# Kernel optimization log

Hardware: AMD Instinct MI355X
Metric: run time of the kernel (lower is better)

The kernel has to match this reference:

```python
import jax, jax.numpy as jnp
import numpy as np

B, S, D, V = 2, 2048, 4096, 32000

def setup_inputs() -> dict:
    key = jax.random.key(0)
    k1, k2, k3 = jax.random.split(key, 3)
    hidden_states = jax.random.normal(k1, (B, S, D), dtype=jnp.float32)
    W = jax.random.normal(k2, (V, D), dtype=jnp.float32) * 0.02  # lm_head weight [vocab, hidden]
    label_ids = jax.random.randint(k3, (B, S), 0, V, dtype=jnp.int64)
    return {"hidden_states": hidden_states, "W": W, "label_ids": label_ids}

def reference(hidden_states, W, label_ids):
    # lm_head: Linear(D, V, bias=False) -> logits [B, S, V], cast to fp32
    logits = jnp.einsum('bsd,vd->bsv', hidden_states, W).astype(jnp.float32)
    # shift: predict token t+1 from position t
    shift_logits = logits[:, :-1, :].reshape(-1, V)          # [B*(S-1), V]
    shift_labels = label_ids[:, 1:].reshape(-1)              # [B*(S-1)]
    logp = jax.nn.log_softmax(shift_logits, axis=-1)
    nll = -jnp.take_along_axis(logp, shift_labels[:, None], axis=1)[:, 0]
    loss = jnp.mean(nll)  # CrossEntropyLoss default reduction='mean'
    return loss, logits
```

## Files before the change

kernel.cpp:

```cpp
#include <hip/hip_runtime.h>
#include <hip/hip_bf16.h>

#define M_ 4096
#define N_ 32000
#define K_ 4096
#define S_ 2048
#define SM1 2047
#define NROWS 4094
#define NT_ 64
#define NB_ 125

typedef __bf16 bf16x8 __attribute__((ext_vector_type(8)));
typedef float f32x4 __attribute__((ext_vector_type(4)));

#define GLDS16(g, l)                                                         \
  __builtin_amdgcn_global_load_lds(                                          \
      (__attribute__((address_space(1))) const void*)(g),                    \
      (__attribute__((address_space(3))) void*)(l), 16, 0, 0)
#define BAR() __builtin_amdgcn_s_barrier()
#define PRIO1() __builtin_amdgcn_s_setprio(1)
#define PRIO0() __builtin_amdgcn_s_setprio(0)
#define VMCNT(n) asm volatile("s_waitcnt vmcnt(" #n ")" ::: "memory")

__global__ __launch_bounds__(256) void cvt_f32_to_bf16(
    const float* __restrict__ in, bf16x8* __restrict__ out, long n8) {
  long i0 = (long)blockIdx.x * blockDim.x + threadIdx.x;
  long stride = (long)gridDim.x * blockDim.x;
  for (long i = i0; i < n8; i += stride) {
    const float4* p = reinterpret_cast<const float4*>(in) + i * 2;
    float4 a = p[0];
    float4 b = p[1];
    bf16x8 v;
    v[0] = (__bf16)a.x; v[1] = (__bf16)a.y; v[2] = (__bf16)a.z; v[3] = (__bf16)a.w;
    v[4] = (__bf16)b.x; v[5] = (__bf16)b.y; v[6] = (__bf16)b.z; v[7] = (__bf16)b.w;
    out[i] = v;
  }
}

__global__ __launch_bounds__(512, 2) void gemm256(
    const __bf16* __restrict__ A, const __bf16* __restrict__ B,
    float* __restrict__ C, float* __restrict__ pm, float* __restrict__ ps) {
  __shared__ __align__(1024) unsigned char smem[2][65536];

  const int tid = threadIdx.x;
  const int bid = blockIdx.x;
  const int wg = (bid & 7) * 250 + (bid >> 3);
  const int nblk = wg >> 4;
  const int mblk = wg & 15;
  const int m0 = mblk * 256;
  const int n0 = nblk * 256;

  const int w = tid >> 6;
  const int lane = tid & 63;
  const int wm = w >> 2;
  const int wn = w & 3;
  const int rl = lane & 15;
  const int cl = lane >> 4;
  const int srow = tid >> 3;
  const int scc = tid & 7;

  f32x4 acc[8][4];
#pragma unroll
  for (int i = 0; i < 8; ++i)
#pragma unroll
    for (int j = 0; j < 4; ++j) acc[i][j] = (f32x4){0.f, 0.f, 0.f, 0.f};

  auto stA2 = [&](int nbuf, int kt, int q) {
#pragma unroll
    for (int j = 0; j < 2; ++j) {
      const int r0 = q * 64 + j * 128;
      const int row = r0 + srow;
      const int c = scc ^ (row & 7);
      GLDS16(A + (size_t)(m0 + row) * K_ + kt * 64 + c * 8,
             &smem[nbuf][r0 * 128 + tid * 16]);
    }
  };
  auto stB2 = [&](int nbuf, int kt, int q) {
#pragma unroll
    for (int j = 0; j < 2; ++j) {
      const int cg = j * 512 + tid;
      const int rl_ = cg >> 3;
      const int row = ((rl_ >> 5) << 6) + q * 32 + (rl_ & 31);
      const int cc = cg & 7;
      const int c = cc ^ (row & 7);
      GLDS16(B + (size_t)(n0 + row) * K_ + kt * 64 + c * 8,
             &smem[nbuf][32768 + row * 128 + cc * 16]);
    }
  };
  auto ld = [&](const unsigned char* base, int row, int c) -> bf16x8 {
    return *(const bf16x8*)(base + row * 128 + (((c ^ row) & 7) << 4));
  };

  stA2(0, 0, 0); stB2(0, 0, 0); stA2(0, 0, 1); stB2(0, 0, 1);
  VMCNT(4);
  BAR();

  bf16x8 al[4][2], ah[4][2], b0r[2][2], b1r[2][2];
#pragma unroll
  for (int jj = 0; jj < 2; ++jj)
#pragma unroll
    for (int ks = 0; ks < 2; ++ks)
      b0r[jj][ks] = ld(smem[0] + 32768, wn * 64 + jj * 16 + rl, ks * 4 + cl);
#pragma unroll
  for (int ii = 0; ii < 4; ++ii)
#pragma unroll
    for (int ks = 0; ks < 2; ++ks)
      al[ii][ks] = ld(smem[0], wm * 128 + ii * 16 + rl, ks * 4 + cl);

  for (int s = 0; s < NT_; ++s) {
    const int cur = s & 1;
    const int nxt = cur ^ 1;
    const unsigned char* bA = smem[cur];
    const unsigned char* bB = smem[cur] + 32768;
    const bool st = (s + 1 < NT_);

    if (st) stA2(nxt, s + 1, 0);
    PRIO1();
#pragma unroll
    for (int ii = 0; ii < 4; ++ii)
#pragma unroll
      for (int jj = 0; jj < 2; ++jj)
#pragma unroll
        for (int ks = 0; ks < 2; ++ks)
          acc[ii][jj] = __builtin_amdgcn_mfma_f32_16x16x32_bf16(
              al[ii][ks], b0r[jj][ks], acc[ii][jj], 0, 0, 0);
    PRIO0();
    if (st) { VMCNT(2); } else { VMCNT(0); }
    BAR();

    if (st) stB2(nxt, s + 1, 0);
#pragma unroll
    for (int jj = 0; jj < 2; ++jj)
#pragma unroll
      for (int ks = 0; ks < 2; ++ks)
        b1r[jj][ks] = ld(bB, wn * 64 + 32 + jj * 16 + rl, ks * 4 + cl);
#pragma unroll
    for (int ii = 0; ii < 4; ++ii)
#pragma unroll
      for (int ks = 0; ks < 2; ++ks)
        ah[ii][ks] = ld(bA, wm * 128 + 64 + ii * 16 + rl, ks * 4 + cl);
    PRIO1();
#pragma unroll
    for (int ii = 0; ii < 4; ++ii)
#pragma unroll
      for (int jj = 0; jj < 2; ++jj)
#pragma unroll
        for (int ks = 0; ks < 2; ++ks)
          acc[ii][2 + jj] = __builtin_amdgcn_mfma_f32_16x16x32_bf16(
              al[ii][ks], b1r[jj][ks], acc[ii][2 + jj], 0, 0, 0);
    PRIO0();
    BAR();

    if (st) stA2(nxt, s + 1, 1);
    PRIO1();
#pragma unroll
    for (int ii = 0; ii < 4; ++ii)
#pragma unroll
      for (int jj = 0; jj < 2; ++jj)
#pragma unroll
        for (int ks = 0; ks < 2; ++ks)
          acc[4 + ii][jj] = __builtin_amdgcn_mfma_f32_16x16x32_bf16(
              ah[ii][ks], b0r[jj][ks], acc[4 + ii][jj], 0, 0, 0);
    PRIO0();
    BAR();

    if (st) stB2(nxt, s + 1, 1);
    PRIO1();
#pragma unroll
    for (int ii = 0; ii < 4; ++ii)
#pragma unroll
      for (int jj = 0; jj < 2; ++jj)
#pragma unroll
        for (int ks = 0; ks < 2; ++ks)
          acc[4 + ii][2 + jj] = __builtin_amdgcn_mfma_f32_16x16x32_bf16(
              ah[ii][ks], b1r[jj][ks], acc[4 + ii][2 + jj], 0, 0, 0);
    PRIO0();
    if (st) VMCNT(4);
    BAR();
    if (st) {
      const unsigned char* nA = smem[nxt];
      const unsigned char* nB = smem[nxt] + 32768;
#pragma unroll
      for (int jj = 0; jj < 2; ++jj)
#pragma unroll
        for (int ks = 0; ks < 2; ++ks)
          b0r[jj][ks] = ld(nB, wn * 64 + jj * 16 + rl, ks * 4 + cl);
#pragma unroll
      for (int ii = 0; ii < 4; ++ii)
#pragma unroll
        for (int ks = 0; ks < 2; ++ks)
          al[ii][ks] = ld(nA, wm * 128 + ii * 16 + rl, ks * 4 + cl);
    }
  }

  float* red = (float*)smem;
  float* red2 = (float*)(smem[0] + 4096);
  {
    BAR();
#pragma unroll
    for (int i = 0; i < 8; ++i)
#pragma unroll
      for (int r = 0; r < 4; ++r) {
        float v = fmaxf(fmaxf(acc[i][0][r], acc[i][1][r]),
                        fmaxf(acc[i][2][r], acc[i][3][r]));
#pragma unroll
        for (int o = 1; o < 16; o <<= 1) v = fmaxf(v, __shfl_xor(v, o));
        if (rl == 0) red[wn * 256 + wm * 128 + i * 16 + cl * 4 + r] = v;
      }
    BAR();
#pragma unroll
    for (int i = 0; i < 8; ++i)
#pragma unroll
      for (int r = 0; r < 4; ++r) {
        const int row = wm * 128 + i * 16 + cl * 4 + r;
        const float mx = fmaxf(fmaxf(red[row], red[256 + row]),
                               fmaxf(red[512 + row], red[768 + row]));
        float sv = __expf(acc[i][0][r] - mx) + __expf(acc[i][1][r] - mx) +
                   __expf(acc[i][2][r] - mx) + __expf(acc[i][3][r] - mx);
#pragma unroll
        for (int o = 1; o < 16; o <<= 1) sv += __shfl_xor(sv, o);
        if (rl == 0) red2[wn * 256 + row] = sv;
      }
    BAR();
    if (tid < 256) {
      const int row = tid;
      const float Mv = fmaxf(fmaxf(red[row], red[256 + row]),
                             fmaxf(red[512 + row], red[768 + row]));
      const float Sv = red2[row] + red2[256 + row] + red2[512 + row] +
                       red2[768 + row];
      pm[(size_t)(m0 + row) * NB_ + nblk] = Mv;
      ps[(size_t)(m0 + row) * NB_ + nblk] = Sv;
    }
  }

#pragma unroll
  for (int i = 0; i < 8; ++i)
#pragma unroll
    for (int j = 0; j < 4; ++j)
#pragma unroll
      for (int r = 0; r < 4; ++r) {
        const int grow = m0 + wm * 128 + i * 16 + cl * 4 + r;
        const int gcol = n0 + wn * 64 + j * 16 + rl;
        C[(size_t)grow * N_ + gcol] = acc[i][j][r];
      }
}

__global__ __launch_bounds__(64) void ce_combine(
    const float* __restrict__ pm, const float* __restrict__ ps,
    const float* __restrict__ logits, const int* __restrict__ labels,
    float* __restrict__ nll) {
  const int r = blockIdx.x;
  const int b = r / SM1;
  const int t = r - b * SM1;
  const int m = b * S_ + t;
  const int lane = threadIdx.x;
  float M = -3.4e38f, Ssum = 0.f;
  for (int j = lane; j < NB_; j += 64) {
    const float mj = pm[(size_t)m * NB_ + j];
    const float sj = ps[(size_t)m * NB_ + j];
    if (mj > M) { Ssum *= __expf(M - mj); M = mj; }
    Ssum += sj * __expf(mj - M);
  }
#pragma unroll
  for (int o = 32; o > 0; o >>= 1) {
    const float M2 = __shfl_xor(M, o), S2 = __shfl_xor(Ssum, o);
    const float mn = fmaxf(M, M2);
    Ssum = Ssum * __expf(M - mn) + S2 * __expf(M2 - mn);
    M = mn;
  }
  if (lane == 0) {
    const int lbl = labels[b * S_ + t + 1];
    nll[r] = M + __logf(Ssum) - logits[(size_t)m * N_ + lbl];
  }
}

__global__ __launch_bounds__(256) void gemm_fb(const float* __restrict__ Ap,
                                               const float* __restrict__ Bp,
                                               float* __restrict__ Cp) {
  __shared__ __align__(1024) unsigned char smem[2][16384];
  const int tid = threadIdx.x;
  const int bid = blockIdx.x;
  const int swz = (bid & 7) * 1000 + (bid >> 3);
  const int nblk = swz >> 5;
  const int mblk = swz & 31;
  const int m0 = mblk * 128;
  const int n0 = nblk * 128;
  const int w = tid >> 6, lane = tid & 63;
  const int wm = w >> 1, wn = w & 1;
  const int rl = lane & 15, cl = lane >> 4;

  f32x4 acc[4][4];
#pragma unroll
  for (int i = 0; i < 4; ++i)
#pragma unroll
    for (int j = 0; j < 4; ++j) acc[i][j] = (f32x4){0.f, 0.f, 0.f, 0.f};

  auto stage = [&](int buf, int kt) {
    const int k0 = kt * 32;
#pragma unroll
    for (int j = 0; j < 2; ++j) {
      const int t = j * 256 + tid;
      const int row = t >> 2;
      const int c = t & 3;
      const int rp = row >> 1;
      const int pp = ((row & 1) * 4 + c) ^ (rp & 7);
      const int lb = rp * 128 + pp * 16;
      {
        const float4* g = (const float4*)(Ap + (size_t)(m0 + row) * K_ + k0 + c * 8);
        float4 x = g[0], y = g[1];
        bf16x8 v;
        v[0] = (__bf16)x.x; v[1] = (__bf16)x.y; v[2] = (__bf16)x.z; v[3] = (__bf16)x.w;
        v[4] = (__bf16)y.x; v[5] = (__bf16)y.y; v[6] = (__bf16)y.z; v[7] = (__bf16)y.w;
        *(bf16x8*)(&smem[buf][lb]) = v;
      }
      {
        const float4* g = (const float4*)(Bp + (size_t)(n0 + row) * K_ + k0 + c * 8);
        float4 x = g[0], y = g[1];
        bf16x8 v;
        v[0] = (__bf16)x.x; v[1] = (__bf16)x.y; v[2] = (__bf16)x.z; v[3] = (__bf16)x.w;
        v[4] = (__bf16)y.x; v[5] = (__bf16)y.y; v[6] = (__bf16)y.z; v[7] = (__bf16)y.w;
        *(bf16x8*)(&smem[buf][8192 + lb]) = v;
      }
    }
  };
  auto ldfrag = [&](const unsigned char* base, int row, int c) -> bf16x8 {
    const int rp = row >> 1;
    const int pp = ((row & 1) * 4 + c) ^ (rp & 7);
    return *(const bf16x8*)(base + rp * 128 + pp * 16);
  };
  auto compute = [&](int buf) {
    const unsigned char* bA = smem[buf];
    const unsigned char* bB = smem[buf] + 8192;
    bf16x8 af[4], bfv[4];
#pragma unroll
    for (int i = 0; i < 4; ++i) af[i] = ldfrag(bA, wm * 64 + i * 16 + rl, cl);
#pragma unroll
    for (int j = 0; j < 4; ++j) bfv[j] = ldfrag(bB, wn * 64 + j * 16 + rl, cl);
#pragma unroll
    for (int i = 0; i < 4; ++i)
#pragma unroll
      for (int j = 0; j < 4; ++j)
        acc[i][j] = __builtin_amdgcn_mfma_f32_16x16x32_bf16(af[i], bfv[j],
                                                            acc[i][j], 0, 0, 0);
  };

  stage(0, 0);
  __syncthreads();
  for (int kt = 0; kt < 128; kt += 2) {
    if (kt + 1 < 128) stage(1, kt + 1);
    compute(0);
    __syncthreads();
    if (kt + 2 < 128) stage(0, kt + 2);
    compute(1);
    __syncthreads();
  }
#pragma unroll
  for (int i = 0; i < 4; ++i)
#pragma unroll
    for (int j = 0; j < 4; ++j)
#pragma unroll
      for (int r = 0; r < 4; ++r) {
        const int grow = m0 + wm * 64 + i * 16 + cl * 4 + r;
        const int gcol = n0 + wn * 64 + j * 16 + rl;
        Cp[(size_t)grow * N_ + gcol] = acc[i][j][r];
      }
}

__global__ __launch_bounds__(256) void ce_rows(const float* __restrict__ logits,
                                               const int* __restrict__ labels,
                                               float* __restrict__ nll) {
  const int r = blockIdx.x;
  const int b = r / SM1;
  const int t = r - b * SM1;
  const float* row = logits + (size_t)(b * S_ + t) * N_;
  float m = -3.4e38f, s = 0.f;
  const float4* row4 = (const float4*)row;
  for (int i = threadIdx.x; i < 7936; i += 256) {
    float4 v = row4[i];
    float mx = fmaxf(fmaxf(v.x, v.y), fmaxf(v.z, v.w));
    if (mx > m) { s *= __expf(m - mx); m = mx; }
    s += __expf(v.x - m) + __expf(v.y - m) + __expf(v.z - m) + __expf(v.w - m);
  }
  {
    float v = row[31744 + threadIdx.x];
    if (v > m) { s *= __expf(m - v); m = v; }
    s += __expf(v - m);
  }
#pragma unroll
  for (int o = 32; o > 0; o >>= 1) {
    float m2 = __shfl_xor(m, o), s2 = __shfl_xor(s, o);
    float mn = fmaxf(m, m2);
    s = s * __expf(m - mn) + s2 * __expf(m2 - mn);
    m = mn;
  }
  __shared__ float rm[4], rs[4];
  if ((threadIdx.x & 63) == 0) { rm[threadIdx.x >> 6] = m; rs[threadIdx.x >> 6] = s; }
  __syncthreads();
  if (threadIdx.x == 0) {
    float M = fmaxf(fmaxf(rm[0], rm[1]), fmaxf(rm[2], rm[3]));
    float S = rs[0] * __expf(rm[0] - M) + rs[1] * __expf(rm[1] - M) +
              rs[2] * __expf(rm[2] - M) + rs[3] * __expf(rm[3] - M);
    nll[r] = M + __logf(S) - row[labels[b * S_ + t + 1]];
  }
}

__global__ __launch_bounds__(256) void reduce_loss(const float* __restrict__ nll,
                                                   float* __restrict__ out) {
  float s = 0.f;
  for (int i = threadIdx.x; i < NROWS; i += 256) s += nll[i];
#pragma unroll
  for (int o = 32; o > 0; o >>= 1) s += __shfl_xor(s, o);
  __shared__ float sb[4];
  if ((threadIdx.x & 63) == 0) sb[threadIdx.x >> 6] = s;
  __syncthreads();
  if (threadIdx.x == 0) out[0] = (sb[0] + sb[1] + sb[2] + sb[3]) / (float)NROWS;
}

extern "C" void kernel_launch(void* const* d_in, const int* in_sizes, int n_in,
                              void* d_out, int out_size, void* d_ws,
                              size_t ws_size, hipStream_t stream) {
  const float* h = (const float*)d_in[0];
  const float* Wf = (const float*)d_in[1];
  const int* labels = (const int*)d_in[2];
  float* out = (float*)d_out;
  float* logits = out + 1;

  const size_t abytes = (size_t)M_ * K_ * 2;
  const size_t bbytes = (size_t)N_ * K_ * 2;
  const size_t pbytes = (size_t)M_ * NB_ * 4;
  const size_t need = abytes + bbytes + 2 * pbytes + (size_t)NROWS * 4;

  if (ws_size >= need) {
    unsigned char* base = (unsigned char*)d_ws;
    __bf16* hA = (__bf16*)base;
    __bf16* wB = (__bf16*)(base + abytes);
    float* pm = (float*)(base + abytes + bbytes);
    float* psum = (float*)(base + abytes + bbytes + pbytes);
    float* nll = (float*)(base + abytes + bbytes + 2 * pbytes);
    cvt_f32_to_bf16<<<2048, 256, 0, stream>>>(h, (bf16x8*)hA,
                                              (long)((size_t)M_ * K_ / 8));
    cvt_f32_to_bf16<<<4096, 256, 0, stream>>>(Wf, (bf16x8*)wB,
                                              (long)((size_t)N_ * K_ / 8));
    gemm256<<<2000, 512, 0, stream>>>(hA, wB, logits, pm, psum);
    ce_combine<<<NROWS, 64, 0, stream>>>(pm, psum, logits, labels, nll);
    reduce_loss<<<1, 256, 0, stream>>>(nll, out);
  } else {
    float* nll = (float*)d_ws;
    gemm_fb<<<8000, 256, 0, stream>>>(h, Wf, logits);
    ce_rows<<<4094, 256, 0, stream>>>(logits, labels, nll);
    reduce_loss<<<1, 256, 0, stream>>>(nll, out);
  }
}
```

Baseline: 1.214 ms.

## Deepen GEMM global-to-LDS prefetch to two k-tiles ahead

Restructures the main GEMM loop so global_load_lds for tile s+2 is issued into the buffer being consumed, interleaved with the four MFMA quadrants, with vmcnt waits allowing about six outstanding loads. LDS fragment reads move to the start of each phase, guarded by barriers and lgkmcnt(0) waits. The aim is to hide more global-memory latency behind the MFMA work. In exchange it adds extra barriers per iteration and relies on tight buffer-reuse ordering, which risks races or extra stalls.

```diff
diff --git a/kernel.cpp b/kernel.cpp
--- a/kernel.cpp
+++ b/kernel.cpp
@@ -21,6 +21,7 @@
 #define PRIO1() __builtin_amdgcn_s_setprio(1)
 #define PRIO0() __builtin_amdgcn_s_setprio(0)
 #define VMCNT(n) asm volatile("s_waitcnt vmcnt(" #n ")" ::: "memory")
+#define LGKM0() asm volatile("s_waitcnt lgkmcnt(0)" ::: "memory")
 
 __global__ __launch_bounds__(256) void cvt_f32_to_bf16(
     const float* __restrict__ in, bf16x8* __restrict__ out, long n8) {
@@ -93,28 +94,33 @@
 
   stA2(0, 0, 0); stB2(0, 0, 0); stA2(0, 0, 1); stB2(0, 0, 1);
   VMCNT(4);
+  stA2(1, 1, 0); stB2(1, 1, 0); stA2(1, 1, 1);
+  VMCNT(6);
   BAR();
 
   bf16x8 al[4][2], ah[4][2], b0r[2][2], b1r[2][2];
-#pragma unroll
-  for (int jj = 0; jj < 2; ++jj)
-#pragma unroll
-    for (int ks = 0; ks < 2; ++ks)
-      b0r[jj][ks] = ld(smem[0] + 32768, wn * 64 + jj * 16 + rl, ks * 4 + cl);
-#pragma unroll
-  for (int ii = 0; ii < 4; ++ii)
-#pragma unroll
-    for (int ks = 0; ks < 2; ++ks)
-      al[ii][ks] = ld(smem[0], wm * 128 + ii * 16 + rl, ks * 4 + cl);
 
   for (int s = 0; s < NT_; ++s) {
     const int cur = s & 1;
     const int nxt = cur ^ 1;
     const unsigned char* bA = smem[cur];
     const unsigned char* bB = smem[cur] + 32768;
-    const bool st = (s + 1 < NT_);
-
-    if (st) stA2(nxt, s + 1, 0);
+    const bool s1 = (s + 1 < NT_);
+    const bool s2 = (s + 2 < NT_);
+
+#pragma unroll
+    for (int jj = 0; jj < 2; ++jj)
+#pragma unroll
+      for (int ks = 0; ks < 2; ++ks)
+        b0r[jj][ks] = ld(bB, wn * 64 + jj * 16 + rl, ks * 4 + cl);
+#pragma unroll
+    for (int ii = 0; ii < 4; ++ii)
+#pragma unroll
+      for (int ks = 0; ks < 2; ++ks)
+        al[ii][ks] = ld(bA, wm * 128 + ii * 16 + rl, ks * 4 + cl);
+    if (s1) stB2(nxt, s + 1, 1);
+    BAR();
+    LGKM0();
     PRIO1();
 #pragma unroll
     for (int ii = 0; ii < 4; ++ii)
@@ -125,20 +131,16 @@
           acc[ii][jj] = __builtin_amdgcn_mfma_f32_16x16x32_bf16(
               al[ii][ks], b0r[jj][ks], acc[ii][jj], 0, 0, 0);
     PRIO0();
-    if (st) { VMCNT(2); } else { VMCNT(0); }
-    BAR();
-
-    if (st) stB2(nxt, s + 1, 0);
+    BAR();
+
 #pragma unroll
     for (int jj = 0; jj < 2; ++jj)
 #pragma unroll
       for (int ks = 0; ks < 2; ++ks)
         b1r[jj][ks] = ld(bB, wn * 64 + 32 + jj * 16 + rl, ks * 4 + cl);
-#pragma unroll
-    for (int ii = 0; ii < 4; ++ii)
-#pragma unroll
-      for (int ks = 0; ks < 2; ++ks)
-        ah[ii][ks] = ld(bA, wm * 128 + 64 + ii * 16 + rl, ks * 4 + cl);
+    if (s2) stA2(cur, s + 2, 0);
+    BAR();
+    LGKM0();
     PRIO1();
 #pragma unroll
     for (int ii = 0; ii < 4; ++ii)
@@ -151,7 +153,14 @@
     PRIO0();
     BAR();
 
-    if (st) stA2(nxt, s + 1, 1);
+#pragma unroll
+    for (int ii = 0; ii < 4; ++ii)
+#pragma unroll
+      for (int ks = 0; ks < 2; ++ks)
+        ah[ii][ks] = ld(bA, wm * 128 + 64 + ii * 16 + rl, ks * 4 + cl);
+    if (s2) stB2(cur, s + 2, 0);
+    BAR();
+    LGKM0();
     PRIO1();
 #pragma unroll
     for (int ii = 0; ii < 4; ++ii)
@@ -164,7 +173,8 @@
     PRIO0();
     BAR();
 
-    if (st) stB2(nxt, s + 1, 1);
+    if (s2) stA2(cur, s + 2, 1);
+    BAR();
     PRIO1();
 #pragma unroll
     for (int ii = 0; ii < 4; ++ii)
@@ -175,22 +185,10 @@
           acc[4 + ii][2 + jj] = __builtin_amdgcn_mfma_f32_16x16x32_bf16(
               ah[ii][ks], b1r[jj][ks], acc[4 + ii][2 + jj], 0, 0, 0);
     PRIO0();
-    if (st) VMCNT(4);
-    BAR();
-    if (st) {
-      const unsigned char* nA = smem[nxt];
-      const unsigned char* nB = smem[nxt] + 32768;
-#pragma unroll
-      for (int jj = 0; jj < 2; ++jj)
-#pragma unroll
-        for (int ks = 0; ks < 2; ++ks)
-          b0r[jj][ks] = ld(nB, wn * 64 + jj * 16 + rl, ks * 4 + cl);
-#pragma unroll
-      for (int ii = 0; ii < 4; ++ii)
-#pragma unroll
-        for (int ks = 0; ks < 2; ++ks)
-          al[ii][ks] = ld(nA, wm * 128 + ii * 16 + rl, ks * 4 + cl);
+    if (s1) {
+      if (s2) { VMCNT(6); } else { VMCNT(0); }
     }
+    BAR();
   }
 
   float* red = (float*)smem;
```

Result: no change. 1.208 ms (-0.5%).
